# Kernel tuning notes

Hardware: AMD Instinct MI355X
Metric: run time of the kernel (lower is better)

## Reference

```python
import jax, jax.numpy as jnp
import numpy as np
from jax import lax

T, H, I, E = 1024, 1024, 512, 16          # tokens, hidden, moe_intermediate, n_routed_experts
TOP_K, N_GROUP, TOPK_GROUP = 4, 4, 2
N_SHARED = 2
I_SHARED = I * N_SHARED                    # shared-expert intermediate size
ROUTED_SCALE = 2.5


def setup_inputs() -> dict:
    key = jax.random.key(0)
    ks = jax.random.split(key, 9)
    s = lambda k, shape, fan: jax.random.normal(k, shape, jnp.float32) * (fan ** -0.5)
    return {
        "hidden_states": jax.random.normal(ks[0], (T, H), jnp.float32),
        "router_w": s(ks[1], (H, E), H),                 # gate: ReplicatedLinear(H, E)
        "e_bias": jax.random.normal(ks[2], (E,), jnp.float32) * 0.01,  # e_score_correction_bias
        "w_gate": s(ks[3], (E, H, I), H),                # routed experts gate_proj
        "w_up": s(ks[4], (E, H, I), H),                  # routed experts up_proj
        "w_down": s(ks[5], (E, I, H), I),                # routed experts down_proj
        "sw_gate": s(ks[6], (H, I_SHARED), H),           # shared experts gate_proj
        "sw_up": s(ks[7], (H, I_SHARED), H),             # shared experts up_proj
        "sw_down": s(ks[8], (I_SHARED, H), I_SHARED),    # shared experts down_proj
    }


def _grouped_topk_sigmoid(logits, e_bias):
    # DeepSeek-V3 'noaux_tc' grouped top-k with sigmoid scoring.
    scores = jax.nn.sigmoid(logits)                      # [T, E]
    sc = scores + e_bias                                 # biased scores for selection only
    g = sc.reshape(-1, N_GROUP, E // N_GROUP)
    group_scores = lax.top_k(g, 2)[0].sum(-1)            # [T, n_group]: sum of top-2 per group
    _, gidx = lax.top_k(group_scores, TOPK_GROUP)        # [T, topk_group]
    gmask = jax.nn.one_hot(gidx, N_GROUP, dtype=sc.dtype).sum(1)  # [T, n_group]
    emask = jnp.repeat(gmask, E // N_GROUP, axis=1)      # [T, E]
    masked = jnp.where(emask > 0, sc, 0.0)               # sigmoid scores are >=0
    _, tidx = lax.top_k(masked, TOP_K)                   # [T, top_k]
    w = jnp.take_along_axis(scores, tidx, axis=1)        # weights use UNbiased scores
    w = w / (w.sum(-1, keepdims=True) + 1e-20)           # norm_topk_prob=True
    # dense combine weights [T, E]
    combine = (jax.nn.one_hot(tidx, E, dtype=w.dtype) * w[..., None]).sum(1)
    return combine


def reference(hidden_states, router_w, e_bias, w_gate, w_up, w_down,
              sw_gate, sw_up, sw_down):
    x = hidden_states                                    # [T, H]
    logits = x @ router_w                                # [T, E]
    combine = _grouped_topk_sigmoid(logits, e_bias)      # [T, E]

    # routed experts: SiLU-gated MLP per expert, dense-over-experts reference
    gp = jnp.einsum('th,ehi->tei', x, w_gate)            # [T, E, I]
    up = jnp.einsum('th,ehi->tei', x, w_up)
    h = jax.nn.silu(gp) * up
    oe = jnp.einsum('tei,eih->teh', h, w_down)           # [T, E, H]
    routed = jnp.einsum('teh,te->th', oe, combine)       # [T, H]

    # shared experts MLP (reduce_results=False path), fp32 path scales routed only
    shared = (jax.nn.silu(x @ sw_gate) * (x @ sw_up)) @ sw_down  # [T, H]
    return routed * ROUTED_SCALE + shared
```

## Files before the change

### kernel.cpp

```cpp
#include <hip/hip_runtime.h>
#include <stdint.h>

#define T_TOK 1024
#define HDIM  1024
#define IDIM  512
#define NEXP  16
#define ISH   1024
#define MAXT128  48
#define HSLOTS   6144
#define NSCHED   (MAXT128 * 8)
#define NCVT     6912

typedef _Float16 f16;
typedef __attribute__((ext_vector_type(8))) _Float16 f16x8;
typedef __attribute__((ext_vector_type(4))) _Float16 f16x4;
typedef __attribute__((ext_vector_type(4))) float    f32x4;

__device__ __forceinline__ void gld16(const void* g, void* l) {
  __builtin_amdgcn_global_load_lds(
      (__attribute__((address_space(1))) void*)(uintptr_t)g,
      (__attribute__((address_space(3))) void*)(uint32_t)(uintptr_t)l,
      16, 0, 0);
}

__device__ __forceinline__ f16x8 ldsfrag(const f16* buf, int row, int lch) {
  int phys = lch ^ (row & 7);
  return *(const f16x8*)(buf + row * 64 + phys * 8);
}

__global__ __launch_bounds__(256) void cvt_kernel(
    const float* __restrict__ wg, const float* __restrict__ wu, const float* __restrict__ wd,
    const float* __restrict__ sg, const float* __restrict__ su, const float* __restrict__ sd,
    f16* __restrict__ wgt, f16* __restrict__ wut, f16* __restrict__ wdt,
    f16* __restrict__ sgt, f16* __restrict__ sut, f16* __restrict__ sdt) {
  int b = blockIdx.x;
  const float* src; f16* dst; int R, C, tr, tc;
  if (b < 4096) {
    int w = b >> 11, e = (b >> 7) & 15, t2 = b & 127;
    tr = t2 >> 3; tc = t2 & 7;
    R = 1024; C = 512;
    src = (w ? wu : wg) + (size_t)e * HDIM * IDIM;
    dst = (w ? wut : wgt) + (size_t)e * HDIM * IDIM;
  } else if (b < 6144) {
    int e = (b - 4096) >> 7, t2 = b & 127;
    tr = t2 >> 4; tc = t2 & 15;
    R = 512; C = 1024;
    src = wd + (size_t)e * HDIM * IDIM;
    dst = wdt + (size_t)e * HDIM * IDIM;
  } else {
    int w = (b - 6144) >> 8, t2 = b & 255;
    tr = t2 >> 4; tc = t2 & 15;
    R = 1024; C = 1024;
    src = (w == 0) ? sg : (w == 1 ? su : sd);
    dst = (w == 0) ? sgt : (w == 1 ? sut : sdt);
  }
  __shared__ f16 tile[64 * 72];
  int t = threadIdx.x;
#pragma unroll
  for (int j = 0; j < 4; j++) {
    int lin = t + 256 * j;
    int row = lin >> 4, cc = lin & 15;
    float4 v = *(const float4*)(src + (size_t)(tr * 64 + row) * C + tc * 64 + cc * 4);
    f16x4 h = { (f16)v.x, (f16)v.y, (f16)v.z, (f16)v.w };
    *(f16x4*)(tile + row * 72 + cc * 4) = h;
  }
  __syncthreads();
#pragma unroll
  for (int j = 0; j < 2; j++) {
    int lin = t + 256 * j;
    int n = lin >> 3, c3 = lin & 7;
    f16x8 o;
#pragma unroll
    for (int i = 0; i < 8; i++) o[i] = tile[(c3 * 8 + i) * 72 + n];
    *(f16x8*)(dst + (size_t)(tc * 64 + n) * R + tr * 64 + c3 * 8) = o;
  }
}

__global__ __launch_bounds__(256) void router_kernel(
    const float* __restrict__ x, const float* __restrict__ rw, const float* __restrict__ ebias,
    f16* __restrict__ xh, int* __restrict__ topk_i, float* __restrict__ topk_w) {
  int wave = threadIdx.x >> 6, l = threadIdx.x & 63;
  int t = blockIdx.x * 4 + wave;
  float acc[16];
#pragma unroll
  for (int e = 0; e < 16; e++) acc[e] = 0.f;
#pragma unroll
  for (int i = 0; i < 4; i++) {
    int k = i * 256 + l * 4;
    float4 xv = *(const float4*)(x + (size_t)t * HDIM + k);
    f16x4 h = { (f16)xv.x, (f16)xv.y, (f16)xv.z, (f16)xv.w };
    *(f16x4*)(xh + (size_t)t * HDIM + k) = h;
    const float* xp = &xv.x;
#pragma unroll
    for (int j = 0; j < 4; j++) {
      float xj = xp[j];
      const float4* w4 = (const float4*)(rw + (size_t)(k + j) * 16);
#pragma unroll
      for (int q = 0; q < 4; q++) {
        float4 w = w4[q];
        acc[q*4+0] += xj * w.x; acc[q*4+1] += xj * w.y;
        acc[q*4+2] += xj * w.z; acc[q*4+3] += xj * w.w;
      }
    }
  }
#pragma unroll
  for (int off = 32; off >= 1; off >>= 1)
#pragma unroll
    for (int e = 0; e < 16; e++) acc[e] += __shfl_xor(acc[e], off, 64);

  if (l == 0) {
    float s[16], sc[16];
#pragma unroll
    for (int e = 0; e < 16; e++) {
      s[e] = 1.f / (1.f + __expf(-acc[e]));
      sc[e] = s[e] + ebias[e];
    }
    float gs[4];
#pragma unroll
    for (int g = 0; g < 4; g++) {
      float a = -1e30f, b2 = -1e30f;
#pragma unroll
      for (int j = 0; j < 4; j++) {
        float v = sc[g*4 + j];
        if (v > a) { b2 = a; a = v; } else if (v > b2) { b2 = v; }
      }
      gs[g] = a + b2;
    }
    int g1 = 0;
    for (int g = 1; g < 4; g++) if (gs[g] > gs[g1]) g1 = g;
    int g2 = -1;
    for (int g = 0; g < 4; g++) if (g != g1 && (g2 < 0 || gs[g] > gs[g2])) g2 = g;
    float masked[16];
#pragma unroll
    for (int e = 0; e < 16; e++) {
      int g = e >> 2;
      masked[e] = (g == g1 || g == g2) ? sc[e] : 0.0f;
    }
    int idx[4]; float wv[4]; float denom = 1e-20f;
#pragma unroll
    for (int j = 0; j < 4; j++) {
      int best = 0; float bv = masked[0];
      for (int e = 1; e < 16; e++) if (masked[e] > bv) { bv = masked[e]; best = e; }
      idx[j] = best; wv[j] = s[best]; denom += s[best];
      masked[best] = -1e30f;
    }
#pragma unroll
    for (int j = 0; j < 4; j++) {
      topk_i[t * 4 + j] = idx[j];
      topk_w[t * 4 + j] = wv[j] / denom * 2.5f;
    }
  }
}

__global__ __launch_bounds__(1024) void scatter_kernel(
    const int* __restrict__ tki,
    int* __restrict__ tok, int* __restrict__ slotmap,
    int* __restrict__ tile_e, int* __restrict__ tile_srow,
    int* __restrict__ tile_hb, int* __restrict__ ntl, int* __restrict__ sched) {
  __shared__ int lcnt[NEXP], lpos[NEXP], lbase[NEXP];
  int t = threadIdx.x;
  if (t < NEXP) { lcnt[t] = 0; lpos[t] = 0; }
  if (t < NSCHED) sched[t] = -1;
  __syncthreads();
  int idx[4];
#pragma unroll
  for (int j = 0; j < 4; j++) idx[j] = tki[t*4+j];
#pragma unroll
  for (int j = 0; j < 4; j++) atomicAdd(&lcnt[idx[j]], 1);
  __syncthreads();
  if (t == 0) {
    int total = 0, slots = 0;
    int sc[8];
    for (int q = 0; q < 8; q++) sc[q] = 0;
    for (int e = 0; e < NEXP; e++) {
      int c = lcnt[e], nt = (c + 127) >> 7;
      lbase[e] = slots;
      for (int j = 0; j < nt; j++) {
        tile_e[total] = e; tile_srow[total] = j * 128; tile_hb[total] = slots + j * 128;
        int x = e & 7;
        if (sc[x] + 8 > MAXT128) {
          int bx = 0;
          for (int q = 1; q < 8; q++) if (sc[q] < sc[bx]) bx = q;
          x = bx;
        }
        for (int n = 0; n < 8; n++) { sched[x + 8 * sc[x]] = total * 8 + n; sc[x]++; }
        total++;
      }
      slots += nt * 128;
    }
    ntl[0] = total;
  }
  __syncthreads();
#pragma unroll
  for (int j = 0; j < 4; j++) {
    int slot = atomicAdd(&lpos[idx[j]], 1);
    tok[idx[j] * T_TOK + slot] = t;
    slotmap[t * 4 + j] = lbase[idx[j]] + slot;
  }
  __syncthreads();
  int e = t >> 6, s = t & 63;
  int c = lcnt[e];
  int top = ((c + 127) >> 7) << 7;
  for (int s2 = c + s; s2 < top; s2 += 64) tok[e * T_TOK + s2] = 0;
}

__device__ __forceinline__ f32x4 mfma16(f16x8 a, f16x8 b, f32x4 c) {
  return __builtin_amdgcn_mfma_f32_16x16x32_f16(a, b, c, 0, 0, 0);
}

__global__ __launch_bounds__(512, 4) void gu_all(
    const f16* __restrict__ xh,
    const f16* __restrict__ sgt, const f16* __restrict__ sut, f16* __restrict__ hsh,
    const f16* __restrict__ wgt, const f16* __restrict__ wut, f16* __restrict__ hbuf,
    const int* __restrict__ tile_e, const int* __restrict__ tile_srow,
    const int* __restrict__ tile_hb, const int* __restrict__ ntl,
    const int* __restrict__ tok, const int* __restrict__ sched) {
  int b = blockIdx.x;
  const f16 *Bg, *Bu; f16* Hdst;
  int e = 0, srow = 0, mbase, n0, N;
  bool gather = (b >= 128);
  if (!gather) {
    int x = b & 7, s = b >> 3;
    Hdst = hsh; N = ISH;
    mbase = (s >> 1) * 128;
    n0 = (x + ((s & 1) << 3)) * 64;
    Bg = sgt + (size_t)n0 * HDIM; Bu = sut + (size_t)n0 * HDIM;
  } else {
    int w = sched[b - 128];
    if (w < 0) return;
    int by = w >> 3;
    e = tile_e[by]; srow = tile_srow[by]; mbase = tile_hb[by];
    Hdst = hbuf; N = IDIM;
    n0 = (w & 7) * 64;
    size_t bo = (size_t)e * HDIM * IDIM + (size_t)n0 * HDIM;
    Bg = wgt + bo; Bu = wut + bo;
  }
  const int K = HDIM;

  __shared__ f16 As[2 * 128 * 64];
  __shared__ f16 Bgs[2 * 64 * 64], Bus[2 * 64 * 64];

  int tid = threadIdx.x, lane = tid & 63, wave = tid >> 6;
  int quad = lane >> 4, l15 = lane & 15;
  int r = lane >> 3, p = lane & 7;
  int kcol = (p ^ r) << 3;

  const f16* gbA[2]; f16* lbA[2];
#pragma unroll
  for (int jj = 0; jj < 2; jj++) {
    int j = wave * 2 + jj;
    int row = j * 8 + r;
    int grow = gather ? tok[e * T_TOK + srow + row] : (mbase + row);
    gbA[jj] = xh + (size_t)grow * K + kcol;
    lbA[jj] = (f16*)As + (j << 9);
  }
  const f16* gbBg = Bg + (size_t)(wave * 8 + r) * K + kcol;
  const f16* gbBu = Bu + (size_t)(wave * 8 + r) * K + kcol;
  f16* lbBg = (f16*)Bgs + (wave << 9);
  f16* lbBu = (f16*)Bus + (wave << 9);

  int wr = wave >> 1, wc = wave & 1;
  f32x4 zero = {0.f, 0.f, 0.f, 0.f};
  f32x4 aG[2][2], aU[2][2];
#pragma unroll
  for (int mi = 0; mi < 2; mi++)
#pragma unroll
    for (int ni = 0; ni < 2; ni++) { aG[mi][ni] = zero; aU[mi][ni] = zero; }

#pragma unroll
  for (int jj = 0; jj < 2; jj++) gld16(gbA[jj], lbA[jj]);
  gld16(gbBg, lbBg);
  gld16(gbBu, lbBu);
  __syncthreads();

  const int nk = K >> 6;
  for (int it = 0; it < nk; ++it) {
    int cb = it & 1, nb = cb ^ 1;
    if (it + 1 < nk) {
      int kt = (it + 1) << 6;
#pragma unroll
      for (int jj = 0; jj < 2; jj++) gld16(gbA[jj] + kt, lbA[jj] + nb * 8192);
      gld16(gbBg + kt, lbBg + nb * 4096);
      gld16(gbBu + kt, lbBu + nb * 4096);
    }
    const f16* Ab = (const f16*)As + cb * 8192;
    const f16* Gb = (const f16*)Bgs + cb * 4096;
    const f16* Ub = (const f16*)Bus + cb * 4096;
#pragma unroll
    for (int ks = 0; ks < 2; ks++) {
      int lch = (ks << 2) + quad;
      f16x8 a[2], g[2], u[2];
#pragma unroll
      for (int mi = 0; mi < 2; mi++) a[mi] = ldsfrag(Ab, 32 * wr + 16 * mi + l15, lch);
#pragma unroll
      for (int ni = 0; ni < 2; ni++) {
        g[ni] = ldsfrag(Gb, 32 * wc + 16 * ni + l15, lch);
        u[ni] = ldsfrag(Ub, 32 * wc + 16 * ni + l15, lch);
      }
#pragma unroll
      for (int mi = 0; mi < 2; mi++)
#pragma unroll
        for (int ni = 0; ni < 2; ni++) {
          aG[mi][ni] = mfma16(a[mi], g[ni], aG[mi][ni]);
          aU[mi][ni] = mfma16(a[mi], u[ni], aU[mi][ni]);
        }
    }
    __syncthreads();
  }
#pragma unroll
  for (int mi = 0; mi < 2; mi++)
#pragma unroll
    for (int ni = 0; ni < 2; ni++)
#pragma unroll
      for (int rg = 0; rg < 4; rg++) {
        int m = 32 * wr + 16 * mi + (quad << 2) + rg;
        int n = n0 + 32 * wc + 16 * ni + l15;
        float g = aG[mi][ni][rg], u = aU[mi][ni][rg];
        float val = (g / (1.f + __expf(-g))) * u;
        Hdst[(size_t)(mbase + m) * N + n] = (f16)val;
      }
}

__global__ __launch_bounds__(512, 4) void down_all(
    const f16* __restrict__ hsh, const f16* __restrict__ sdt,
    const f16* __restrict__ hbuf, const f16* __restrict__ wdt,
    float* __restrict__ out, f16* __restrict__ odown,
    const int* __restrict__ tile_hb, const int* __restrict__ tile_e,
    const int* __restrict__ ntl, const int* __restrict__ sched) {
  int b = blockIdx.x;
  bool routed = (b >= 64);
  const f16* A; const f16* B; int K, abase, n0;
  if (!routed) {
    A = hsh; K = ISH;
    n0 = (b & 7) * 128; abase = (b >> 3) * 128;
    B = sdt + (size_t)n0 * K;
  } else {
    int w = sched[b - 64];
    if (w < 0) return;
    int by = w >> 3;
    abase = tile_hb[by];
    A = hbuf; K = IDIM;
    n0 = (w & 7) * 128;
    B = wdt + (size_t)tile_e[by] * IDIM * HDIM + (size_t)n0 * K;
  }

  __shared__ f16 As[2 * 128 * 64];
  __shared__ f16 Bs[2 * 128 * 64];

  int tid = threadIdx.x, lane = tid & 63, wave = tid >> 6;
  int quad = lane >> 4, l15 = lane & 15;
  int r = lane >> 3, p = lane & 7;
  int kcol = (p ^ r) << 3;

  const f16* gbA[2]; f16* lbA[2];
  const f16* gbB[2]; f16* lbB[2];
#pragma unroll
  for (int jj = 0; jj < 2; jj++) {
    int j = wave * 2 + jj;
    int row = j * 8 + r;
    gbA[jj] = A + (size_t)(abase + row) * K + kcol;
    lbA[jj] = (f16*)As + (j << 9);
    gbB[jj] = B + (size_t)row * K + kcol;
    lbB[jj] = (f16*)Bs + (j << 9);
  }

  int wr = wave >> 1, wc = wave & 1;
  f32x4 zero = {0.f, 0.f, 0.f, 0.f};
  f32x4 ac[2][4];
#pragma unroll
  for (int mi = 0; mi < 2; mi++)
#pragma unroll
    for (int ni = 0; ni < 4; ni++) ac[mi][ni] = zero;

#pragma unroll
  for (int jj = 0; jj < 2; jj++) { gld16(gbA[jj], lbA[jj]); gld16(gbB[jj], lbB[jj]); }
  __syncthreads();

  const int nk = K >> 6;
  for (int it = 0; it < nk; ++it) {
    int cb = it & 1, nb = cb ^ 1;
    if (it + 1 < nk) {
      int kt = (it + 1) << 6;
#pragma unroll
      for (int jj = 0; jj < 2; jj++) {
        gld16(gbA[jj] + kt, lbA[jj] + nb * 8192);
        gld16(gbB[jj] + kt, lbB[jj] + nb * 8192);
      }
    }
    const f16* Ab = (const f16*)As + cb * 8192;
    const f16* Bb = (const f16*)Bs + cb * 8192;
#pragma unroll
    for (int ks = 0; ks < 2; ks++) {
      int lch = (ks << 2) + quad;
      f16x8 a[2], bb[4];
#pragma unroll
      for (int mi = 0; mi < 2; mi++) a[mi] = ldsfrag(Ab, 32 * wr + 16 * mi + l15, lch);
#pragma unroll
      for (int ni = 0; ni < 4; ni++) bb[ni] = ldsfrag(Bb, 64 * wc + 16 * ni + l15, lch);
#pragma unroll
      for (int mi = 0; mi < 2; mi++)
#pragma unroll
        for (int ni = 0; ni < 4; ni++)
          ac[mi][ni] = mfma16(a[mi], bb[ni], ac[mi][ni]);
    }
    __syncthreads();
  }
#pragma unroll
  for (int mi = 0; mi < 2; mi++)
#pragma unroll
    for (int ni = 0; ni < 4; ni++)
#pragma unroll
      for (int rg = 0; rg < 4; rg++) {
        int m = 32 * wr + 16 * mi + (quad << 2) + rg;
        int n = n0 + 64 * wc + 16 * ni + l15;
        if (routed) odown[(size_t)(abase + m) * HDIM + n] = (f16)ac[mi][ni][rg];
        else        out  [(size_t)(abase + m) * HDIM + n] = ac[mi][ni][rg];
      }
}

__global__ __launch_bounds__(256) void combine_kernel(
    const f16* __restrict__ odown, const int* __restrict__ slotmap,
    const float* __restrict__ tkw, float* __restrict__ out) {
  int t = blockIdx.x;
  __shared__ int ss[4]; __shared__ float sw[4];
  if (threadIdx.x < 4) {
    ss[threadIdx.x] = slotmap[t * 4 + threadIdx.x];
    sw[threadIdx.x] = tkw[t * 4 + threadIdx.x];
  }
  __syncthreads();
  int h = threadIdx.x * 4;
  float4 acc = *(const float4*)(out + (size_t)t * HDIM + h);
#pragma unroll
  for (int j = 0; j < 4; j++) {
    f16x4 v = *(const f16x4*)(odown + (size_t)ss[j] * HDIM + h);
    float wj = sw[j];
    acc.x += wj * (float)v[0]; acc.y += wj * (float)v[1];
    acc.z += wj * (float)v[2]; acc.w += wj * (float)v[3];
  }
  *(float4*)(out + (size_t)t * HDIM + h) = acc;
}

extern "C" void kernel_launch(void* const* d_in, const int* in_sizes, int n_in,
                              void* d_out, int out_size, void* d_ws, size_t ws_size,
                              hipStream_t stream) {
  const float* x  = (const float*)d_in[0];
  const float* rw = (const float*)d_in[1];
  const float* eb = (const float*)d_in[2];
  const float* wg = (const float*)d_in[3];
  const float* wu = (const float*)d_in[4];
  const float* wd = (const float*)d_in[5];
  const float* sg = (const float*)d_in[6];
  const float* su = (const float*)d_in[7];
  const float* sd = (const float*)d_in[8];
  float* out = (float*)d_out;
  (void)in_sizes; (void)n_in; (void)out_size; (void)ws_size;

  char* w = (char*)d_ws;
  size_t off = 0;
  auto alloc = [&](size_t b) { void* p = w + off; off = (off + b + 255) & ~(size_t)255; return p; };

  f16* xh   = (f16*)alloc((size_t)T_TOK * HDIM * 2);
  f16* hbuf = (f16*)alloc((size_t)HSLOTS * IDIM * 2);
  f16* hsh  = (f16*)alloc((size_t)T_TOK * ISH * 2);
  f16* odown = (f16*)alloc((size_t)HSLOTS * HDIM * 2);
  f16* wgt  = (f16*)alloc((size_t)NEXP * HDIM * IDIM * 2);
  f16* wut  = (f16*)alloc((size_t)NEXP * HDIM * IDIM * 2);
  f16* wdt  = (f16*)alloc((size_t)NEXP * HDIM * IDIM * 2);
  f16* sgt  = (f16*)alloc((size_t)HDIM * ISH * 2);
  f16* sut  = (f16*)alloc((size_t)HDIM * ISH * 2);
  f16* sdt  = (f16*)alloc((size_t)HDIM * ISH * 2);
  int* topk_i = (int*)alloc((size_t)T_TOK * 4 * 4);
  float* topk_w = (float*)alloc((size_t)T_TOK * 4 * 4);
  int* tok  = (int*)alloc((size_t)NEXP * T_TOK * 4);
  int* slotmap = (int*)alloc((size_t)T_TOK * 4 * 4);
  int* tile_e    = (int*)alloc(MAXT128 * 4);
  int* tile_srow = (int*)alloc(MAXT128 * 4);
  int* tile_hb   = (int*)alloc(MAXT128 * 4);
  int* ntl       = (int*)alloc(16);
  int* sched     = (int*)alloc(NSCHED * 4);

  cvt_kernel<<<NCVT, 256, 0, stream>>>(wg, wu, wd, sg, su, sd,
                                       wgt, wut, wdt, sgt, sut, sdt);
  router_kernel<<<T_TOK / 4, 256, 0, stream>>>(x, rw, eb, xh, topk_i, topk_w);
  scatter_kernel<<<1, 1024, 0, stream>>>(topk_i, tok, slotmap,
                                         tile_e, tile_srow, tile_hb, ntl, sched);
  gu_all<<<128 + NSCHED, 512, 0, stream>>>(
      xh, sgt, sut, hsh, wgt, wut, hbuf, tile_e, tile_srow, tile_hb, ntl, tok, sched);
  down_all<<<64 + NSCHED, 512, 0, stream>>>(
      hsh, sdt, hbuf, wdt, out, odown, tile_hb, tile_e, ntl, sched);
  combine_kernel<<<T_TOK, 256, 0, stream>>>(odown, slotmap, topk_w, out);
}
```

Baseline: 227.7 us.

## Fuse router, scatter and weight conversion; combine via atomic adds in down GEMM

```diff
diff --git a/kernel.cpp b/kernel.cpp
--- a/kernel.cpp
+++ b/kernel.cpp
@@ -10,6 +10,7 @@
 #define HSLOTS   6144
 #define NSCHED   (MAXT128 * 8)
 #define NCVT     6912
+#define NRTB     256
 
 typedef _Float16 f16;
 typedef __attribute__((ext_vector_type(8))) _Float16 f16x8;
@@ -28,147 +29,159 @@
   return *(const f16x8*)(buf + row * 64 + phys * 8);
 }
 
-__global__ __launch_bounds__(256) void cvt_kernel(
+__device__ __forceinline__ f32x4 mfma16(f16x8 a, f16x8 b, f32x4 c) {
+  return __builtin_amdgcn_mfma_f32_16x16x32_f16(a, b, c, 0, 0, 0);
+}
+
+__global__ __launch_bounds__(256) void cvtrt_kernel(
     const float* __restrict__ wg, const float* __restrict__ wu, const float* __restrict__ wd,
     const float* __restrict__ sg, const float* __restrict__ su, const float* __restrict__ sd,
     f16* __restrict__ wgt, f16* __restrict__ wut, f16* __restrict__ wdt,
-    f16* __restrict__ sgt, f16* __restrict__ sut, f16* __restrict__ sdt) {
-  int b = blockIdx.x;
-  const float* src; f16* dst; int R, C, tr, tc;
-  if (b < 4096) {
-    int w = b >> 11, e = (b >> 7) & 15, t2 = b & 127;
-    tr = t2 >> 3; tc = t2 & 7;
-    R = 1024; C = 512;
-    src = (w ? wu : wg) + (size_t)e * HDIM * IDIM;
-    dst = (w ? wut : wgt) + (size_t)e * HDIM * IDIM;
-  } else if (b < 6144) {
-    int e = (b - 4096) >> 7, t2 = b & 127;
-    tr = t2 >> 4; tc = t2 & 15;
-    R = 512; C = 1024;
-    src = wd + (size_t)e * HDIM * IDIM;
-    dst = wdt + (size_t)e * HDIM * IDIM;
-  } else {
-    int w = (b - 6144) >> 8, t2 = b & 255;
-    tr = t2 >> 4; tc = t2 & 15;
-    R = 1024; C = 1024;
-    src = (w == 0) ? sg : (w == 1 ? su : sd);
-    dst = (w == 0) ? sgt : (w == 1 ? sut : sdt);
-  }
-  __shared__ f16 tile[64 * 72];
-  int t = threadIdx.x;
-#pragma unroll
-  for (int j = 0; j < 4; j++) {
-    int lin = t + 256 * j;
-    int row = lin >> 4, cc = lin & 15;
-    float4 v = *(const float4*)(src + (size_t)(tr * 64 + row) * C + tc * 64 + cc * 4);
-    f16x4 h = { (f16)v.x, (f16)v.y, (f16)v.z, (f16)v.w };
-    *(f16x4*)(tile + row * 72 + cc * 4) = h;
-  }
-  __syncthreads();
-#pragma unroll
-  for (int j = 0; j < 2; j++) {
-    int lin = t + 256 * j;
-    int n = lin >> 3, c3 = lin & 7;
-    f16x8 o;
-#pragma unroll
-    for (int i = 0; i < 8; i++) o[i] = tile[(c3 * 8 + i) * 72 + n];
-    *(f16x8*)(dst + (size_t)(tc * 64 + n) * R + tr * 64 + c3 * 8) = o;
-  }
-}
-
-__global__ __launch_bounds__(256) void router_kernel(
+    f16* __restrict__ sgt, f16* __restrict__ sut, f16* __restrict__ sdt,
     const float* __restrict__ x, const float* __restrict__ rw, const float* __restrict__ ebias,
-    f16* __restrict__ xh, int* __restrict__ topk_i, float* __restrict__ topk_w) {
-  int wave = threadIdx.x >> 6, l = threadIdx.x & 63;
-  int t = blockIdx.x * 4 + wave;
-  float acc[16];
-#pragma unroll
-  for (int e = 0; e < 16; e++) acc[e] = 0.f;
-#pragma unroll
-  for (int i = 0; i < 4; i++) {
-    int k = i * 256 + l * 4;
-    float4 xv = *(const float4*)(x + (size_t)t * HDIM + k);
-    f16x4 h = { (f16)xv.x, (f16)xv.y, (f16)xv.z, (f16)xv.w };
-    *(f16x4*)(xh + (size_t)t * HDIM + k) = h;
-    const float* xp = &xv.x;
-#pragma unroll
-    for (int j = 0; j < 4; j++) {
-      float xj = xp[j];
-      const float4* w4 = (const float4*)(rw + (size_t)(k + j) * 16);
-#pragma unroll
-      for (int q = 0; q < 4; q++) {
-        float4 w = w4[q];
-        acc[q*4+0] += xj * w.x; acc[q*4+1] += xj * w.y;
-        acc[q*4+2] += xj * w.z; acc[q*4+3] += xj * w.w;
-      }
-    }
-  }
-#pragma unroll
-  for (int off = 32; off >= 1; off >>= 1)
-#pragma unroll
-    for (int e = 0; e < 16; e++) acc[e] += __shfl_xor(acc[e], off, 64);
-
-  if (l == 0) {
-    float s[16], sc[16];
-#pragma unroll
-    for (int e = 0; e < 16; e++) {
-      s[e] = 1.f / (1.f + __expf(-acc[e]));
-      sc[e] = s[e] + ebias[e];
-    }
-    float gs[4];
-#pragma unroll
-    for (int g = 0; g < 4; g++) {
-      float a = -1e30f, b2 = -1e30f;
-#pragma unroll
-      for (int j = 0; j < 4; j++) {
-        float v = sc[g*4 + j];
-        if (v > a) { b2 = a; a = v; } else if (v > b2) { b2 = v; }
-      }
-      gs[g] = a + b2;
-    }
-    int g1 = 0;
-    for (int g = 1; g < 4; g++) if (gs[g] > gs[g1]) g1 = g;
-    int g2 = -1;
-    for (int g = 0; g < 4; g++) if (g != g1 && (g2 < 0 || gs[g] > gs[g2])) g2 = g;
-    float masked[16];
-#pragma unroll
-    for (int e = 0; e < 16; e++) {
-      int g = e >> 2;
-      masked[e] = (g == g1 || g == g2) ? sc[e] : 0.0f;
-    }
-    int idx[4]; float wv[4]; float denom = 1e-20f;
-#pragma unroll
-    for (int j = 0; j < 4; j++) {
-      int best = 0; float bv = masked[0];
-      for (int e = 1; e < 16; e++) if (masked[e] > bv) { bv = masked[e]; best = e; }
-      idx[j] = best; wv[j] = s[best]; denom += s[best];
-      masked[best] = -1e30f;
-    }
-#pragma unroll
-    for (int j = 0; j < 4; j++) {
-      topk_i[t * 4 + j] = idx[j];
-      topk_w[t * 4 + j] = wv[j] / denom * 2.5f;
-    }
-  }
-}
-
-__global__ __launch_bounds__(1024) void scatter_kernel(
-    const int* __restrict__ tki,
-    int* __restrict__ tok, int* __restrict__ slotmap,
+    f16* __restrict__ xh, int* __restrict__ topk_i, float* __restrict__ topk_w,
+    int* __restrict__ ticket,
+    int* __restrict__ tok, float* __restrict__ wslot,
     int* __restrict__ tile_e, int* __restrict__ tile_srow,
     int* __restrict__ tile_hb, int* __restrict__ ntl, int* __restrict__ sched) {
+  int b = blockIdx.x;
+  int tid = threadIdx.x;
+  if (b >= NRTB) {
+    int ub = b - NRTB;
+    __shared__ f16 tile[64 * 72];
+    const float* src; f16* dst; int R, C, tr, tc;
+    if (ub < 4096) {
+      int w = ub >> 11, e = (ub >> 7) & 15, t2 = ub & 127;
+      tr = t2 >> 3; tc = t2 & 7; R = 1024; C = 512;
+      src = (w ? wu : wg) + (size_t)e * HDIM * IDIM;
+      dst = (w ? wut : wgt) + (size_t)e * HDIM * IDIM;
+    } else if (ub < 6144) {
+      int e = (ub - 4096) >> 7, t2 = ub & 127;
+      tr = t2 >> 4; tc = t2 & 15; R = 512; C = 1024;
+      src = wd + (size_t)e * HDIM * IDIM;
+      dst = wdt + (size_t)e * HDIM * IDIM;
+    } else {
+      int w = (ub - 6144) >> 8, t2 = ub & 255;
+      tr = t2 >> 4; tc = t2 & 15; R = 1024; C = 1024;
+      src = (w == 0) ? sg : (w == 1 ? su : sd);
+      dst = (w == 0) ? sgt : (w == 1 ? sut : sdt);
+    }
+#pragma unroll
+    for (int j = 0; j < 4; j++) {
+      int lin = tid + 256 * j;
+      int row = lin >> 4, cc = lin & 15;
+      float4 v = *(const float4*)(src + (size_t)(tr * 64 + row) * C + tc * 64 + cc * 4);
+      f16x4 h = { (f16)v.x, (f16)v.y, (f16)v.z, (f16)v.w };
+      *(f16x4*)(tile + row * 72 + cc * 4) = h;
+    }
+    __syncthreads();
+#pragma unroll
+    for (int j = 0; j < 2; j++) {
+      int lin = tid + 256 * j;
+      int n = lin >> 3, c3 = lin & 7;
+      f16x8 o;
+#pragma unroll
+      for (int i = 0; i < 8; i++) o[i] = tile[(c3 * 8 + i) * 72 + n];
+      *(f16x8*)(dst + (size_t)(tc * 64 + n) * R + tr * 64 + c3 * 8) = o;
+    }
+    return;
+  }
+  {
+    int wave = tid >> 6, l = tid & 63;
+    int t = b * 4 + wave;
+    float acc[16];
+#pragma unroll
+    for (int e = 0; e < 16; e++) acc[e] = 0.f;
+#pragma unroll
+    for (int i = 0; i < 4; i++) {
+      int k = i * 256 + l * 4;
+      float4 xv = *(const float4*)(x + (size_t)t * HDIM + k);
+      f16x4 h = { (f16)xv.x, (f16)xv.y, (f16)xv.z, (f16)xv.w };
+      *(f16x4*)(xh + (size_t)t * HDIM + k) = h;
+      const float* xp = &xv.x;
+#pragma unroll
+      for (int j = 0; j < 4; j++) {
+        float xj = xp[j];
+        const float4* w4 = (const float4*)(rw + (size_t)(k + j) * 16);
+#pragma unroll
+        for (int q = 0; q < 4; q++) {
+          float4 w = w4[q];
+          acc[q*4+0] += xj * w.x; acc[q*4+1] += xj * w.y;
+          acc[q*4+2] += xj * w.z; acc[q*4+3] += xj * w.w;
+        }
+      }
+    }
+#pragma unroll
+    for (int off = 32; off >= 1; off >>= 1)
+#pragma unroll
+      for (int e = 0; e < 16; e++) acc[e] += __shfl_xor(acc[e], off, 64);
+
+    if (l == 0) {
+      float s[16], sc[16];
+#pragma unroll
+      for (int e = 0; e < 16; e++) {
+        s[e] = 1.f / (1.f + __expf(-acc[e]));
+        sc[e] = s[e] + ebias[e];
+      }
+      float gs[4];
+#pragma unroll
+      for (int g = 0; g < 4; g++) {
+        float a = -1e30f, b2 = -1e30f;
+#pragma unroll
+        for (int j = 0; j < 4; j++) {
+          float v = sc[g*4 + j];
+          if (v > a) { b2 = a; a = v; } else if (v > b2) { b2 = v; }
+        }
+        gs[g] = a + b2;
+      }
+      int g1 = 0;
+      for (int g = 1; g < 4; g++) if (gs[g] > gs[g1]) g1 = g;
+      int g2 = -1;
+      for (int g = 0; g < 4; g++) if (g != g1 && (g2 < 0 || gs[g] > gs[g2])) g2 = g;
+      float masked[16];
+#pragma unroll
+      for (int e = 0; e < 16; e++) {
+        int g = e >> 2;
+        masked[e] = (g == g1 || g == g2) ? sc[e] : 0.0f;
+      }
+      int idx[4]; float wv[4]; float denom = 1e-20f;
+#pragma unroll
+      for (int j = 0; j < 4; j++) {
+        int best = 0; float bv = masked[0];
+        for (int e = 1; e < 16; e++) if (masked[e] > bv) { bv = masked[e]; best = e; }
+        idx[j] = best; wv[j] = s[best]; denom += s[best];
+        masked[best] = -1e30f;
+      }
+#pragma unroll
+      for (int j = 0; j < 4; j++) {
+        topk_i[t * 4 + j] = idx[j];
+        topk_w[t * 4 + j] = wv[j] / denom * 2.5f;
+      }
+    }
+  }
+  __shared__ int elect;
+  __threadfence();
+  __syncthreads();
+  if (tid == 0) elect = atomicAdd(ticket, 1);
+  __syncthreads();
+  if (elect != NRTB - 1) return;
+
   __shared__ int lcnt[NEXP], lpos[NEXP], lbase[NEXP];
-  int t = threadIdx.x;
-  if (t < NEXP) { lcnt[t] = 0; lpos[t] = 0; }
-  if (t < NSCHED) sched[t] = -1;
-  __syncthreads();
-  int idx[4];
-#pragma unroll
-  for (int j = 0; j < 4; j++) idx[j] = tki[t*4+j];
-#pragma unroll
-  for (int j = 0; j < 4; j++) atomicAdd(&lcnt[idx[j]], 1);
-  __syncthreads();
-  if (t == 0) {
+  if (tid < NEXP) { lcnt[tid] = 0; lpos[tid] = 0; }
+  for (int s = tid; s < NSCHED; s += 256) sched[s] = -1;
+  __syncthreads();
+  int idx4[4][4];
+#pragma unroll
+  for (int h = 0; h < 4; h++) {
+    int t = h * 256 + tid;
+#pragma unroll
+    for (int j = 0; j < 4; j++) {
+      idx4[h][j] = topk_i[t * 4 + j];
+      atomicAdd(&lcnt[idx4[h][j]], 1);
+    }
+  }
+  __syncthreads();
+  if (tid == 0) {
     int total = 0, slots = 0;
     int sc[8];
     for (int q = 0; q < 8; q++) sc[q] = 0;
@@ -177,13 +190,13 @@
       lbase[e] = slots;
       for (int j = 0; j < nt; j++) {
         tile_e[total] = e; tile_srow[total] = j * 128; tile_hb[total] = slots + j * 128;
-        int x = e & 7;
-        if (sc[x] + 8 > MAXT128) {
+        int x2 = e & 7;
+        if (sc[x2] + 8 > MAXT128) {
           int bx = 0;
           for (int q = 1; q < 8; q++) if (sc[q] < sc[bx]) bx = q;
-          x = bx;
+          x2 = bx;
         }
-        for (int n = 0; n < 8; n++) { sched[x + 8 * sc[x]] = total * 8 + n; sc[x]++; }
+        for (int n = 0; n < 8; n++) { sched[x2 + 8 * sc[x2]] = total * 8 + n; sc[x2]++; }
         total++;
       }
       slots += nt * 128;
@@ -192,20 +205,26 @@
   }
   __syncthreads();
 #pragma unroll
-  for (int j = 0; j < 4; j++) {
-    int slot = atomicAdd(&lpos[idx[j]], 1);
-    tok[idx[j] * T_TOK + slot] = t;
-    slotmap[t * 4 + j] = lbase[idx[j]] + slot;
-  }
-  __syncthreads();
-  int e = t >> 6, s = t & 63;
-  int c = lcnt[e];
-  int top = ((c + 127) >> 7) << 7;
-  for (int s2 = c + s; s2 < top; s2 += 64) tok[e * T_TOK + s2] = 0;
-}
-
-__device__ __forceinline__ f32x4 mfma16(f16x8 a, f16x8 b, f32x4 c) {
-  return __builtin_amdgcn_mfma_f32_16x16x32_f16(a, b, c, 0, 0, 0);
+  for (int h = 0; h < 4; h++) {
+    int t = h * 256 + tid;
+#pragma unroll
+    for (int j = 0; j < 4; j++) {
+      int e = idx4[h][j];
+      int slot = atomicAdd(&lpos[e], 1);
+      tok[e * T_TOK + slot] = t;
+      wslot[lbase[e] + slot] = topk_w[t * 4 + j];
+    }
+  }
+  __syncthreads();
+  for (int t = tid; t < T_TOK; t += 256) {
+    int e = t >> 6, s = t & 63;
+    int c = lcnt[e];
+    int top = ((c + 127) >> 7) << 7;
+    for (int s2 = c + s; s2 < top; s2 += 64) {
+      tok[e * T_TOK + s2] = 0;
+      wslot[lbase[e] + s2] = 0.f;
+    }
+  }
 }
 
 __global__ __launch_bounds__(512, 4) void gu_all(
@@ -324,12 +343,14 @@
 __global__ __launch_bounds__(512, 4) void down_all(
     const f16* __restrict__ hsh, const f16* __restrict__ sdt,
     const f16* __restrict__ hbuf, const f16* __restrict__ wdt,
-    float* __restrict__ out, f16* __restrict__ odown,
+    float* __restrict__ out,
     const int* __restrict__ tile_hb, const int* __restrict__ tile_e,
-    const int* __restrict__ ntl, const int* __restrict__ sched) {
+    const int* __restrict__ tile_srow, const int* __restrict__ ntl,
+    const int* __restrict__ sched,
+    const int* __restrict__ tok, const float* __restrict__ wslot) {
   int b = blockIdx.x;
   bool routed = (b >= 64);
-  const f16* A; const f16* B; int K, abase, n0;
+  const f16* A; const f16* B; int K, abase, n0, e = 0, srow = 0;
   if (!routed) {
     A = hsh; K = ISH;
     n0 = (b & 7) * 128; abase = (b >> 3) * 128;
@@ -338,10 +359,10 @@
     int w = sched[b - 64];
     if (w < 0) return;
     int by = w >> 3;
-    abase = tile_hb[by];
+    abase = tile_hb[by]; e = tile_e[by]; srow = tile_srow[by];
     A = hbuf; K = IDIM;
     n0 = (w & 7) * 128;
-    B = wdt + (size_t)tile_e[by] * IDIM * HDIM + (size_t)n0 * K;
+    B = wdt + (size_t)e * IDIM * HDIM + (size_t)n0 * K;
   }
 
   __shared__ f16 As[2 * 128 * 64];
@@ -408,36 +429,24 @@
 #pragma unroll
   for (int mi = 0; mi < 2; mi++)
 #pragma unroll
-    for (int ni = 0; ni < 4; ni++)
-#pragma unroll
-      for (int rg = 0; rg < 4; rg++) {
-        int m = 32 * wr + 16 * mi + (quad << 2) + rg;
-        int n = n0 + 64 * wc + 16 * ni + l15;
-        if (routed) odown[(size_t)(abase + m) * HDIM + n] = (f16)ac[mi][ni][rg];
-        else        out  [(size_t)(abase + m) * HDIM + n] = ac[mi][ni][rg];
-      }
-}
-
-__global__ __launch_bounds__(256) void combine_kernel(
-    const f16* __restrict__ odown, const int* __restrict__ slotmap,
-    const float* __restrict__ tkw, float* __restrict__ out) {
-  int t = blockIdx.x;
-  __shared__ int ss[4]; __shared__ float sw[4];
-  if (threadIdx.x < 4) {
-    ss[threadIdx.x] = slotmap[t * 4 + threadIdx.x];
-    sw[threadIdx.x] = tkw[t * 4 + threadIdx.x];
-  }
-  __syncthreads();
-  int h = threadIdx.x * 4;
-  float4 acc = *(const float4*)(out + (size_t)t * HDIM + h);
-#pragma unroll
-  for (int j = 0; j < 4; j++) {
-    f16x4 v = *(const f16x4*)(odown + (size_t)ss[j] * HDIM + h);
-    float wj = sw[j];
-    acc.x += wj * (float)v[0]; acc.y += wj * (float)v[1];
-    acc.z += wj * (float)v[2]; acc.w += wj * (float)v[3];
-  }
-  *(float4*)(out + (size_t)t * HDIM + h) = acc;
+    for (int rg = 0; rg < 4; rg++) {
+      int m = 32 * wr + 16 * mi + (quad << 2) + rg;
+      if (routed) {
+        int token = tok[e * T_TOK + srow + m];
+        float wj = wslot[abase + m];
+#pragma unroll
+        for (int ni = 0; ni < 4; ni++) {
+          int n = n0 + 64 * wc + 16 * ni + l15;
+          atomicAdd(&out[(size_t)token * HDIM + n], wj * ac[mi][ni][rg]);
+        }
+      } else {
+#pragma unroll
+        for (int ni = 0; ni < 4; ni++) {
+          int n = n0 + 64 * wc + 16 * ni + l15;
+          atomicAdd(&out[(size_t)(abase + m) * HDIM + n], ac[mi][ni][rg]);
+        }
+      }
+    }
 }
 
 extern "C" void kernel_launch(void* const* d_in, const int* in_sizes, int n_in,
@@ -462,7 +471,6 @@
   f16* xh   = (f16*)alloc((size_t)T_TOK * HDIM * 2);
   f16* hbuf = (f16*)alloc((size_t)HSLOTS * IDIM * 2);
   f16* hsh  = (f16*)alloc((size_t)T_TOK * ISH * 2);
-  f16* odown = (f16*)alloc((size_t)HSLOTS * HDIM * 2);
   f16* wgt  = (f16*)alloc((size_t)NEXP * HDIM * IDIM * 2);
   f16* wut  = (f16*)alloc((size_t)NEXP * HDIM * IDIM * 2);
   f16* wdt  = (f16*)alloc((size_t)NEXP * HDIM * IDIM * 2);
@@ -472,21 +480,23 @@
   int* topk_i = (int*)alloc((size_t)T_TOK * 4 * 4);
   float* topk_w = (float*)alloc((size_t)T_TOK * 4 * 4);
   int* tok  = (int*)alloc((size_t)NEXP * T_TOK * 4);
-  int* slotmap = (int*)alloc((size_t)T_TOK * 4 * 4);
+  float* wslot = (float*)alloc((size_t)HSLOTS * 4);
   int* tile_e    = (int*)alloc(MAXT128 * 4);
   int* tile_srow = (int*)alloc(MAXT128 * 4);
   int* tile_hb   = (int*)alloc(MAXT128 * 4);
   int* ntl       = (int*)alloc(16);
   int* sched     = (int*)alloc(NSCHED * 4);
-
-  cvt_kernel<<<NCVT, 256, 0, stream>>>(wg, wu, wd, sg, su, sd,
-                                       wgt, wut, wdt, sgt, sut, sdt);
-  router_kernel<<<T_TOK / 4, 256, 0, stream>>>(x, rw, eb, xh, topk_i, topk_w);
-  scatter_kernel<<<1, 1024, 0, stream>>>(topk_i, tok, slotmap,
-                                         tile_e, tile_srow, tile_hb, ntl, sched);
+  int* ticket    = (int*)alloc(16);
+
+  hipMemsetAsync(ticket, 0, 4, stream);
+  hipMemsetAsync(out, 0, (size_t)T_TOK * HDIM * 4, stream);
+
+  cvtrt_kernel<<<NRTB + NCVT, 256, 0, stream>>>(
+      wg, wu, wd, sg, su, sd, wgt, wut, wdt, sgt, sut, sdt,
+      x, rw, eb, xh, topk_i, topk_w,
+      ticket, tok, wslot, tile_e, tile_srow, tile_hb, ntl, sched);
   gu_all<<<128 + NSCHED, 512, 0, stream>>>(
       xh, sgt, sut, hsh, wgt, wut, hbuf, tile_e, tile_srow, tile_hb, ntl, tok, sched);
   down_all<<<64 + NSCHED, 512, 0, stream>>>(
-      hsh, sdt, hbuf, wdt, out, odown, tile_hb, tile_e, ntl, sched);
-  combine_kernel<<<T_TOK, 256, 0, stream>>>(odown, slotmap, topk_w, out);
-}
+      hsh, sdt, hbuf, wdt, out, tile_hb, tile_e, tile_srow, ntl, sched, tok, wslot);
+}
```

Result: slower. 350.8 us (+54.1%).
